# Optimization experiments

Hardware: AMD Instinct MI355X
Metric: run time of the kernel (lower is better)

Reference implementation:

```python
import jax, jax.numpy as jnp
import numpy as np

B, S, P = 2, 1024, 1024          # batch, new tokens, start_pos (cached prefix)
E, H, KV, HD = 2048, 32, 8, 64    # embed, heads, kv groups, head_dim
G = H // KV                       # group size = 4
THETA = 500000.0
CTX = P + S                       # cache/context length = 2048


def _rope_tables(start, seqlen):
    inv_freq = 1.0 / (THETA ** (jnp.arange(0, HD, 2, dtype=jnp.float32) / HD))
    pos = jnp.arange(start, start + seqlen, dtype=jnp.float32)
    freqs = jnp.outer(pos, inv_freq)              # [S, HD/2]
    emb = jnp.concatenate([freqs, freqs], axis=-1)  # [S, HD]
    return jnp.cos(emb), jnp.sin(emb)


def setup_inputs() -> dict:
    key = jax.random.key(0)
    ks = jax.random.split(key, 8)
    x = jax.random.normal(ks[0], (B, S, E), dtype=jnp.float32)
    cos1, sin1 = _rope_tables(P, S)
    cos = jnp.broadcast_to(cos1[None], (B, S, HD))
    sin = jnp.broadcast_to(sin1[None], (B, S, HD))
    # causal-with-offset additive mask: query i (global pos P+i) sees key j <= P+i
    qpos = P + jnp.arange(S)[:, None]
    kpos = jnp.arange(CTX)[None, :]
    mask = jnp.where(kpos <= qpos, 0.0, -1e9).astype(jnp.float32)[None, None]  # [1,1,S,CTX]
    cache_k = jax.random.normal(ks[1], (B, KV, CTX, HD), dtype=jnp.float32)
    cache_v = jax.random.normal(ks[2], (B, KV, CTX, HD), dtype=jnp.float32)
    sc = 0.02
    Wq = jax.random.normal(ks[3], (E, E), dtype=jnp.float32) * sc
    Wk = jax.random.normal(ks[4], (KV * HD, E), dtype=jnp.float32) * sc
    Wv = jax.random.normal(ks[5], (KV * HD, E), dtype=jnp.float32) * sc
    Wo = jax.random.normal(ks[6], (E, E), dtype=jnp.float32) * sc
    return {"x": x, "cos": cos, "sin": sin, "mask": mask,
            "cache_k": cache_k, "cache_v": cache_v,
            "Wq": Wq, "Wk": Wk, "Wv": Wv, "Wo": Wo, "start_pos": P}


def _rotate_half(t):
    t1, t2 = t[..., : HD // 2], t[..., HD // 2:]
    return jnp.concatenate([-t2, t1], axis=-1)


def _apply_rope(t, cos, sin):
    # t: [B, nh, S, HD]; cos/sin: [B, S, HD] -> unsqueeze head dim
    c = cos[:, None]
    s = sin[:, None]
    return t * c + _rotate_half(t) * s


def reference(x, cos, sin, mask, cache_k, cache_v, Wq, Wk, Wv, Wo, start_pos):
    b, s, e = x.shape
    q = (x @ Wq.T).reshape(b, s, H, HD).transpose(0, 2, 1, 3)    # [B,H,S,HD]
    k = (x @ Wk.T).reshape(b, s, KV, HD).transpose(0, 2, 1, 3)   # [B,KV,S,HD]
    v = (x @ Wv.T).reshape(b, s, KV, HD).transpose(0, 2, 1, 3)
    q = _apply_rope(q, cos, sin)
    k = _apply_rope(k, cos, sin)
    ck = cache_k.at[:, :, start_pos:start_pos + s].set(k)
    cv = cache_v.at[:, :, start_pos:start_pos + s].set(v)
    keys = ck[:, :, : start_pos + s]      # [B,KV,T,HD]
    vals = cv[:, :, : start_pos + s]
    # GQA without materializing repeated KV: view q as [B,KV,G,S,HD]
    qg = q.reshape(b, KV, G, s, HD)
    scores = jnp.einsum("bkgsh,bkth->bkgst", qg, keys) / jnp.sqrt(jnp.float32(HD))
    scores = scores + mask[:, :, None]    # broadcast mask over group dim
    probs = jax.nn.softmax(scores.astype(jnp.float32), axis=-1).astype(x.dtype)
    out = jnp.einsum("bkgst,bkth->bkgsh", probs, vals)            # [B,KV,G,S,HD]
    out = out.reshape(b, H, s, HD).transpose(0, 2, 1, 3).reshape(b, s, e)
    return out @ Wo.T
```

## Files before the change

### kernel.cpp

```cpp
#include <hip/hip_runtime.h>
#include <cstddef>

#define B   2
#define S   1024
#define PP  1024
#define CTX 2048
#define E   2048
#define H   32
#define KVH 8
#define HD  64
#define GQ  4
#define NQKV 3072

typedef short s4v  __attribute__((ext_vector_type(4)));
typedef short s8v  __attribute__((ext_vector_type(8)));
typedef float f4v  __attribute__((ext_vector_type(4)));

__device__ __forceinline__ short f2bf(float f) {
  union { float f; unsigned u; } v; v.f = f;
  unsigned r = v.u + 0x7fffu + ((v.u >> 16) & 1u);
  return (short)(r >> 16);
}
__device__ __forceinline__ float bf2f(short h) {
  union { unsigned u; float f; } v; v.u = ((unsigned)(unsigned short)h) << 16;
  return v.f;
}

__device__ __forceinline__ void gl_lds16(const void* g, void* l) {
  __builtin_amdgcn_global_load_lds((const __attribute__((address_space(1))) unsigned*)g,
                                   (__attribute__((address_space(3))) unsigned*)l, 16, 0, 0);
}

__global__ __launch_bounds__(256) void prep(const float* __restrict__ x,
                                            const float* __restrict__ Wq,
                                            const float* __restrict__ Wk,
                                            const float* __restrict__ Wv,
                                            const float* __restrict__ Wo,
                                            const float* __restrict__ ck,
                                            const float* __restrict__ cv,
                                            short* __restrict__ xb,
                                            short* __restrict__ wqkv,
                                            short* __restrict__ wob,
                                            short* __restrict__ keys,
                                            short* __restrict__ vt,
                                            float4* __restrict__ outz) {
  __shared__ short Ts[64][72];
  const int blk = blockIdx.x, tid = threadIdx.x;
  if (blk < 7168) {
    const float* s; short* d; int base;
    if (blk < 2048)      { s = x;  d = xb;             base = blk; }
    else if (blk < 4096) { s = Wq; d = wqkv;           base = blk - 2048; }
    else if (blk < 4608) { s = Wk; d = wqkv + 4194304; base = blk - 4096; }
    else if (blk < 5120) { s = Wv; d = wqkv + 5242880; base = blk - 4608; }
    else                 { s = Wo; d = wob;            base = blk - 5120; }
    int i = (base * 256 + tid) * 8;
    float4 a = *(const float4*)&s[i];
    float4 b = *(const float4*)&s[i + 4];
    s8v o;
    o[0]=f2bf(a.x); o[1]=f2bf(a.y); o[2]=f2bf(a.z); o[3]=f2bf(a.w);
    o[4]=f2bf(b.x); o[5]=f2bf(b.y); o[6]=f2bf(b.z); o[7]=f2bf(b.w);
    *(s8v*)&d[i] = o;
  } else if (blk < 7680) {
    int idx = (blk - 7168) * 256 + tid;
    int bkv = idx >> 13;
    int rem = idx & 8191;
    size_t off = (size_t)bkv * (CTX * HD) + (size_t)rem * 8;
    float4 a = *(const float4*)&ck[off];
    float4 b = *(const float4*)&ck[off + 4];
    s8v o;
    o[0]=f2bf(a.x); o[1]=f2bf(a.y); o[2]=f2bf(a.z); o[3]=f2bf(a.w);
    o[4]=f2bf(b.x); o[5]=f2bf(b.y); o[6]=f2bf(b.z); o[7]=f2bf(b.w);
    *(s8v*)&keys[off] = o;
  } else if (blk < 7936) {
    const int blk2 = blk - 7680;
    const int bkv = blk2 >> 4;
    const int p0  = (blk2 & 15) * 64;
    const float* src = cv + (size_t)bkv * CTX * HD + (size_t)p0 * HD;
    {
      int dq = tid & 15, kb = tid >> 4;
      float4 vv[4];
#pragma unroll
      for (int i = 0; i < 4; i++)
        vv[i] = *(const float4*)&src[(size_t)(kb * 4 + i) * HD + dq * 4];
#pragma unroll
      for (int j = 0; j < 4; j++) {
        s4v p;
        p[0]=f2bf(((const float*)&vv[0])[j]); p[1]=f2bf(((const float*)&vv[1])[j]);
        p[2]=f2bf(((const float*)&vv[2])[j]); p[3]=f2bf(((const float*)&vv[3])[j]);
        *(s4v*)&Ts[dq * 4 + j][kb * 4] = p;
      }
    }
    __syncthreads();
    {
      int d = tid >> 2, c = tid & 3;
      short* dst = vt + ((size_t)bkv * HD + d) * CTX + p0 + (c >> 1) * 32 + (c & 1) * 4;
#pragma unroll
      for (int j = 0; j < 4; j++) {
        s4v q4 = *(const s4v*)&Ts[d][c * 16 + j * 4];
        *(s4v*)&dst[j * 8] = q4;
      }
    }
  } else {
    int i0 = (blk - 7936) * 1024 + tid * 4;
#pragma unroll
    for (int j = 0; j < 4; j++) outz[i0 + j] = make_float4(0.f, 0.f, 0.f, 0.f);
  }
}

__global__ __launch_bounds__(256) void qkv_gemm(const short* __restrict__ A,
                                                const short* __restrict__ Bw,
                                                short* __restrict__ qb,
                                                short* __restrict__ ktmp,
                                                short* __restrict__ vt) {
  __shared__ short As[4096];
  __shared__ short Bs[4096];
  const int tid  = threadIdx.x;
  const int wv   = tid >> 6, lane = tid & 63;
  const int wm   = wv & 1, wn = wv >> 1;
  const int n16  = lane & 15, g = lane >> 4;
  const int m0   = blockIdx.y * 128, n0 = blockIdx.x * 128;
  const int K = 2048;

  const int s0 = tid, s1 = 256 + tid;
  const int r0 = s0 >> 2, c0 = ((s0 & 3) ^ ((r0 >> 1) & 3)) * 8;
  const int r1 = s1 >> 2, c1 = ((s1 & 3) ^ ((r1 >> 1) & 3)) * 8;
  const short* pA0 = A + (size_t)(m0 + r0) * K + c0;
  const short* pA1 = A + (size_t)(m0 + r1) * K + c1;
  const short* pB0 = Bw + (size_t)(n0 + r0) * K + c0;
  const short* pB1 = Bw + (size_t)(n0 + r1) * K + c1;
  short* lA0 = As + (wv * 64) * 8;
  short* lA1 = As + (256 + wv * 64) * 8;
  short* lB0 = Bs + (wv * 64) * 8;
  short* lB1 = Bs + (256 + wv * 64) * 8;

  const int xv = (g ^ ((n16 >> 1) & 3)) * 8;

  f4v acc[4][4] = {};
  for (int k0 = 0; k0 < K; k0 += 32) {
    __syncthreads();
    gl_lds16(pA0, lA0); gl_lds16(pA1, lA1);
    gl_lds16(pB0, lB0); gl_lds16(pB1, lB1);
    pA0 += 32; pA1 += 32; pB0 += 32; pB1 += 32;
    __syncthreads();

    s8v af[4], bf[4];
#pragma unroll
    for (int mt = 0; mt < 4; mt++)
      af[mt] = *(const s8v*)&As[(wm * 64 + mt * 16 + n16) * 32 + xv];
#pragma unroll
    for (int nt = 0; nt < 4; nt++)
      bf[nt] = *(const s8v*)&Bs[(wn * 64 + nt * 16 + n16) * 32 + xv];
#pragma unroll
    for (int mt = 0; mt < 4; mt++)
#pragma unroll
      for (int nt = 0; nt < 4; nt++)
        acc[mt][nt] = __builtin_amdgcn_mfma_f32_16x16x32_bf16(af[mt], bf[nt], acc[mt][nt], 0, 0, 0);
  }

  const int rowb = m0 + wm * 64 + g * 4;
  const int colb = n0 + wn * 64 + n16;
  if (n0 < 2048) {
#pragma unroll
    for (int mt = 0; mt < 4; mt++)
#pragma unroll
      for (int nt = 0; nt < 4; nt++) {
        size_t base = (size_t)(rowb + mt * 16) * E + colb + nt * 16;
#pragma unroll
        for (int r = 0; r < 4; r++)
          qb[base + (size_t)r * E] = f2bf(acc[mt][nt][r]);
      }
  } else if (n0 < 2560) {
#pragma unroll
    for (int mt = 0; mt < 4; mt++)
#pragma unroll
      for (int nt = 0; nt < 4; nt++) {
        size_t base = (size_t)(rowb + mt * 16) * 512 + colb - 2048 + nt * 16;
#pragma unroll
        for (int r = 0; r < 4; r++)
          ktmp[base + (size_t)r * 512] = f2bf(acc[mt][nt][r]);
      }
  } else {
    const int b    = m0 >> 10;
    const int head = ((n0 - 2560) >> 6) + wn;
    const int sbase = (m0 - (b << 10)) + wm * 64;
    const size_t vrowb = (size_t)(b * KVH + head) * HD;
#pragma unroll
    for (int mt = 0; mt < 4; mt++) {
      const int pos = PP + sbase + ((mt >> 1) << 5) + ((mt & 1) << 2) + (g << 3);
#pragma unroll
      for (int nt = 0; nt < 4; nt++) {
        const int d = nt * 16 + n16;
        s4v o;
        o[0] = f2bf(acc[mt][nt][0]); o[1] = f2bf(acc[mt][nt][1]);
        o[2] = f2bf(acc[mt][nt][2]); o[3] = f2bf(acc[mt][nt][3]);
        *(s4v*)&vt[(vrowb + d) * CTX + pos] = o;
      }
    }
  }
}

__global__ __launch_bounds__(256) void gemm_bf16_sk(const short* __restrict__ A,
                                                    const short* __restrict__ Bw,
                                                    float* __restrict__ C,
                                                    int M, int N, int K) {
  __shared__ short As[4096];
  __shared__ short Bs[4096];
  const int tid  = threadIdx.x;
  const int wv   = tid >> 6, lane = tid & 63;
  const int wm   = wv & 1, wn = wv >> 1;
  const int n16  = lane & 15, g = lane >> 4;
  const int m0   = blockIdx.y * 128, n0 = blockIdx.x * 128;
  const int kh   = K >> 1;
  const int kbeg = blockIdx.z * kh;

  const int s0 = tid, s1 = 256 + tid;
  const int r0 = s0 >> 2, c0 = ((s0 & 3) ^ ((r0 >> 1) & 3)) * 8;
  const int r1 = s1 >> 2, c1 = ((s1 & 3) ^ ((r1 >> 1) & 3)) * 8;
  const short* pA0 = A + (size_t)(m0 + r0) * K + kbeg + c0;
  const short* pA1 = A + (size_t)(m0 + r1) * K + kbeg + c1;
  const short* pB0 = Bw + (size_t)(n0 + r0) * K + kbeg + c0;
  const short* pB1 = Bw + (size_t)(n0 + r1) * K + kbeg + c1;
  short* lA0 = As + (wv * 64) * 8;
  short* lA1 = As + (256 + wv * 64) * 8;
  short* lB0 = Bs + (wv * 64) * 8;
  short* lB1 = Bs + (256 + wv * 64) * 8;

  const int xv = (g ^ ((n16 >> 1) & 3)) * 8;

  f4v acc[4][4] = {};
  for (int k0 = 0; k0 < kh; k0 += 32) {
    __syncthreads();
    gl_lds16(pA0, lA0); gl_lds16(pA1, lA1);
    gl_lds16(pB0, lB0); gl_lds16(pB1, lB1);
    pA0 += 32; pA1 += 32; pB0 += 32; pB1 += 32;
    __syncthreads();

    s8v af[4], bf[4];
#pragma unroll
    for (int mt = 0; mt < 4; mt++)
      af[mt] = *(const s8v*)&As[(wm * 64 + mt * 16 + n16) * 32 + xv];
#pragma unroll
    for (int nt = 0; nt < 4; nt++)
      bf[nt] = *(const s8v*)&Bs[(wn * 64 + nt * 16 + n16) * 32 + xv];
#pragma unroll
    for (int mt = 0; mt < 4; mt++)
#pragma unroll
      for (int nt = 0; nt < 4; nt++)
        acc[mt][nt] = __builtin_amdgcn_mfma_f32_16x16x32_bf16(af[mt], bf[nt], acc[mt][nt], 0, 0, 0);
  }

#pragma unroll
  for (int mt = 0; mt < 4; mt++)
#pragma unroll
    for (int nt = 0; nt < 4; nt++) {
      size_t base = (size_t)(m0 + wm * 64 + mt * 16 + g * 4) * N + n0 + wn * 64 + nt * 16 + n16;
#pragma unroll
      for (int r = 0; r < 4; r++)
        unsafeAtomicAdd(&C[base + (size_t)r * N], acc[mt][nt][r]);
    }
}

__global__ __launch_bounds__(256) void rope_kb(const short* __restrict__ ktmp,
                                               const float* __restrict__ cosb,
                                               const float* __restrict__ sinb,
                                               short* __restrict__ keys) {
  int idx = blockIdx.x * 256 + threadIdx.x;
  int d = idx & 31;
  int kv = (idx >> 5) & (KVH - 1);
  int s = (idx >> 8) & (S - 1);
  int b = idx >> 18;
  size_t row = (size_t)b * S + s;
  float c = cosb[row * HD + d];
  float sn = sinb[row * HD + d];
  float k1 = bf2f(ktmp[row * 512 + kv * 64 + d]);
  float k2 = bf2f(ktmp[row * 512 + kv * 64 + d + 32]);
  size_t drow = (((size_t)b * KVH + kv) * CTX + PP + s) * HD;
  keys[drow + d]      = f2bf(k1 * c - k2 * sn);
  keys[drow + d + 32] = f2bf(k2 * c + k1 * sn);
}

__global__ __launch_bounds__(256) void attn_mfma(const short* __restrict__ qb,
                                                 const float* __restrict__ cosb,
                                                 const float* __restrict__ sinb,
                                                 const short* __restrict__ keys,
                                                 const short* __restrict__ valsT,
                                                 short* __restrict__ attn) {
  __shared__ short Ks[4096];
  __shared__ short VTs[4096];

  const int sblk = 15 - (blockIdx.x & 15);
  const int h    = (blockIdx.x >> 4) & (H - 1);
  const int b    = blockIdx.x >> 9;
  const int kv   = h >> 2;
  const int sq0  = sblk * 64;
  const int kend = PP + sq0 + 64;

  const int tid  = threadIdx.x;
  const int w    = tid >> 6;
  const int lane = tid & 63;
  const int n    = lane & 15;
  const int g    = lane >> 4;

  const short* kbase = keys  + ((size_t)b * KVH + kv) * CTX * HD;
  const short* vtb   = valsT + ((size_t)b * KVH + kv) * (size_t)HD * CTX;

  union { s4v h4[2]; s8v v; } qlo, qhi;
  {
    const size_t row = (size_t)b * S + sq0 + w * 16 + n;
    const short* qrow = qb + row * E + h * 64;
    const float* crow = cosb + row * HD;
    const float* srow = sinb + row * HD;
    const float SC = 0.18033688011112042f;
    s8v q0 = *(const s8v*)&qrow[g * 8];
    s8v q1 = *(const s8v*)&qrow[32 + g * 8];
    float cc[8], ss[8];
    *(float4*)&cc[0] = *(const float4*)&crow[g * 8];
    *(float4*)&cc[4] = *(const float4*)&crow[g * 8 + 4];
    *(float4*)&ss[0] = *(const float4*)&srow[g * 8];
    *(float4*)&ss[4] = *(const float4*)&srow[g * 8 + 4];
#pragma unroll
    for (int j = 0; j < 8; j++) {
      float fl = bf2f(q0[j]), fh = bf2f(q1[j]);
      qlo.v[j] = f2bf((fl * cc[j] - fh * ss[j]) * SC);
      qhi.v[j] = f2bf((fh * cc[j] + fl * ss[j]) * SC);
    }
  }

  f4v O[4] = {{0,0,0,0},{0,0,0,0},{0,0,0,0},{0,0,0,0}};
  float la[4] = {0.f, 0.f, 0.f, 0.f};
  const int qp     = PP + sq0 + w * 16 + n;
  const int qmin_w = PP + sq0 + w * 16;

  const int lrow = lane >> 3;
  const int sw   = (lane & 7) ^ lrow;
  const short* kg0 = kbase + (size_t)(w * 8 + lrow) * HD + sw * 8;
  const short* kg1 = kg0 + 32 * HD;
  const short* vg0 = vtb + (size_t)(w * 8 + lrow) * CTX + sw * 8;
  const short* vg1 = vg0 + (size_t)32 * CTX;
  short* kl0 = Ks + w * 512;
  short* kl1 = Ks + 2048 + w * 512;
  short* vl0 = VTs + w * 512;
  short* vl1 = VTs + 2048 + w * 512;

  const int xsl = (g ^ (n & 7)) * 8;

  for (int k0 = 0; k0 < kend; k0 += 64) {
    __syncthreads();
    gl_lds16(kg0 + (size_t)k0 * HD, kl0);
    gl_lds16(kg1 + (size_t)k0 * HD, kl1);
    gl_lds16(vg0 + k0, vl0);
    gl_lds16(vg1 + k0, vl1);
    __syncthreads();

    if (k0 >= qmin_w + 16) continue;

    f4v sc[4];
#pragma unroll
    for (int st = 0; st < 4; st++) {
      const short* krow = &Ks[(st * 16 + n) * 64];
      s8v alo = *(const s8v*)(krow + xsl);
      s8v ahi = *(const s8v*)(krow + (xsl ^ 32));
      f4v z = {0.f, 0.f, 0.f, 0.f};
      z = __builtin_amdgcn_mfma_f32_16x16x32_bf16(alo, qlo.v, z, 0, 0, 0);
      sc[st] = __builtin_amdgcn_mfma_f32_16x16x32_bf16(ahi, qhi.v, z, 0, 0, 0);
    }

    if (k0 + 63 > qmin_w) {
#pragma unroll
      for (int st = 0; st < 4; st++)
#pragma unroll
        for (int r = 0; r < 4; r++) {
          int kpos = k0 + st * 16 + g * 4 + r;
          if (kpos > qp) sc[st][r] = -3e38f;
        }
    }

    union { unsigned u[4]; s8v v; } pb0, pb1;
#pragma unroll
    for (int st = 0; st < 4; st++) {
      float e0 = __builtin_amdgcn_exp2f(sc[st][0]);
      float e1 = __builtin_amdgcn_exp2f(sc[st][1]);
      float e2 = __builtin_amdgcn_exp2f(sc[st][2]);
      float e3 = __builtin_amdgcn_exp2f(sc[st][3]);
      la[0] += e0; la[1] += e1; la[2] += e2; la[3] += e3;
      unsigned w0, w1;
      asm("v_cvt_pk_bf16_f32 %0, %1, %2" : "=v"(w0) : "v"(e0), "v"(e1));
      asm("v_cvt_pk_bf16_f32 %0, %1, %2" : "=v"(w1) : "v"(e2), "v"(e3));
      if (st < 2) { pb0.u[st * 2] = w0; pb0.u[st * 2 + 1] = w1; }
      else        { pb1.u[(st - 2) * 2] = w0; pb1.u[(st - 2) * 2 + 1] = w1; }
    }

#pragma unroll
    for (int dg = 0; dg < 4; dg++) {
      const short* vr = &VTs[(dg * 16 + n) * 64];
      s8v va = *(const s8v*)(vr + xsl);
      s8v vb = *(const s8v*)(vr + (xsl ^ 32));
      O[dg] = __builtin_amdgcn_mfma_f32_16x16x32_bf16(va, pb0.v, O[dg], 0, 0, 0);
      O[dg] = __builtin_amdgcn_mfma_f32_16x16x32_bf16(vb, pb1.v, O[dg], 0, 0, 0);
    }
  }

  float l = (la[0] + la[1]) + (la[2] + la[3]);
  l += __shfl_xor(l, 16);
  l += __shfl_xor(l, 32);
  const float rl = 1.f / l;
  short* orow = attn + ((size_t)b * S + sq0 + w * 16 + n) * E + h * 64;
#pragma unroll
  for (int dg = 0; dg < 4; dg++) {
    s4v o;
    o[0] = f2bf(O[dg][0] * rl); o[1] = f2bf(O[dg][1] * rl);
    o[2] = f2bf(O[dg][2] * rl); o[3] = f2bf(O[dg][3] * rl);
    *(s4v*)&orow[dg * 16 + g * 4] = o;
  }
}

extern "C" void kernel_launch(void* const* d_in, const int* in_sizes, int n_in,
                              void* d_out, int out_size, void* d_ws, size_t ws_size,
                              hipStream_t stream) {
  const float* x       = (const float*)d_in[0];
  const float* cosb    = (const float*)d_in[1];
  const float* sinb    = (const float*)d_in[2];
  const float* cache_k = (const float*)d_in[4];
  const float* cache_v = (const float*)d_in[5];
  const float* Wq      = (const float*)d_in[6];
  const float* Wk      = (const float*)d_in[7];
  const float* Wv      = (const float*)d_in[8];
  const float* Wo      = (const float*)d_in[9];
  float* out = (float*)d_out;

  short* xb    = (short*)d_ws;
  short* wqkv  = xb + 4194304;
  short* wob   = wqkv + 6291456;
  short* keysb = wob + 4194304;
  short* valsT = keysb + 2097152;
  short* aout  = valsT + 2097152;
  short* qb    = aout + 4194304;
  short* ktmp  = qb + 4194304;

  dim3 blk(256);

  prep<<<8960, blk, 0, stream>>>(x, Wq, Wk, Wv, Wo, cache_k, cache_v,
                                 xb, wqkv, wob, keysb, valsT, (float4*)out);

  qkv_gemm<<<dim3(NQKV / 128, (B * S) / 128), blk, 0, stream>>>(xb, wqkv, qb, ktmp, valsT);

  rope_kb<<<(B * S * KVH * 32) / 256, blk, 0, stream>>>(ktmp, cosb, sinb, keysb);

  attn_mfma<<<B * H * (S / 64), blk, 0, stream>>>(qb, cosb, sinb, keysb, valsT, aout);

  gemm_bf16_sk<<<dim3(E / 128, (B * S) / 128, 2), blk, 0, stream>>>(aout, wob, out, B * S, E, E);
}
```

Measured before the change: 276.5 us.

## Pair complementary query blocks per attention block and double-buffer K/V staging

Each attention workgroup now handles two query tiles, a late one and an early one (15-pr and pr), so causal work per block is balanced and each staged K/V tile in LDS serves both tiles. K/V loads move to a double-buffered LDS scheme that prefetches the next tile while the current one is computed, leaving one barrier per iteration. The grid halves to 512 blocks, and register and LDS use roughly double, which may cut occupancy.

```diff
diff --git a/kernel.cpp b/kernel.cpp
--- a/kernel.cpp
+++ b/kernel.cpp
@@ -285,15 +285,16 @@
                                                  const short* __restrict__ keys,
                                                  const short* __restrict__ valsT,
                                                  short* __restrict__ attn) {
-  __shared__ short Ks[4096];
-  __shared__ short VTs[4096];
-
-  const int sblk = 15 - (blockIdx.x & 15);
-  const int h    = (blockIdx.x >> 4) & (H - 1);
-  const int b    = blockIdx.x >> 9;
-  const int kv   = h >> 2;
-  const int sq0  = sblk * 64;
-  const int kend = PP + sq0 + 64;
+  __shared__ short Ks[8192];
+  __shared__ short VTs[8192];
+
+  const int pr = blockIdx.x & 7;
+  const int h  = (blockIdx.x >> 3) & (H - 1);
+  const int b  = blockIdx.x >> 8;
+  const int kv = h >> 2;
+  const int sqA = (15 - pr) * 64;
+  const int sqB = pr * 64;
+  const int kendA = PP + sqA + 64;
 
   const int tid  = threadIdx.x;
   const int w    = tid >> 6;
@@ -304,8 +305,11 @@
   const short* kbase = keys  + ((size_t)b * KVH + kv) * CTX * HD;
   const short* vtb   = valsT + ((size_t)b * KVH + kv) * (size_t)HD * CTX;
 
-  union { s4v h4[2]; s8v v; } qlo, qhi;
-  {
+  union qfrag { s4v h4[2]; s8v v; };
+  union pu    { unsigned u[4]; s8v v; };
+
+  qfrag qloA, qhiA, qloB, qhiB;
+  auto load_q = [&](int sq0, qfrag& qlo, qfrag& qhi) {
     const size_t row = (size_t)b * S + sq0 + w * 16 + n;
     const short* qrow = qb + row * E + h * 64;
     const float* crow = cosb + row * HD;
@@ -324,12 +328,16 @@
       qlo.v[j] = f2bf((fl * cc[j] - fh * ss[j]) * SC);
       qhi.v[j] = f2bf((fh * cc[j] + fl * ss[j]) * SC);
     }
-  }
-
-  f4v O[4] = {{0,0,0,0},{0,0,0,0},{0,0,0,0},{0,0,0,0}};
-  float la[4] = {0.f, 0.f, 0.f, 0.f};
-  const int qp     = PP + sq0 + w * 16 + n;
-  const int qmin_w = PP + sq0 + w * 16;
+  };
+  load_q(sqA, qloA, qhiA);
+  load_q(sqB, qloB, qhiB);
+
+  f4v OA[4] = {{0,0,0,0},{0,0,0,0},{0,0,0,0},{0,0,0,0}};
+  f4v OB[4] = {{0,0,0,0},{0,0,0,0},{0,0,0,0},{0,0,0,0}};
+  float laA[4] = {0.f,0.f,0.f,0.f};
+  float laB[4] = {0.f,0.f,0.f,0.f};
+  const int qpA = PP + sqA + w * 16 + n, qminA = PP + sqA + w * 16;
+  const int qpB = PP + sqB + w * 16 + n, qminB = PP + sqB + w * 16;
 
   const int lrow = lane >> 3;
   const int sw   = (lane & 7) ^ lrow;
@@ -337,45 +345,27 @@
   const short* kg1 = kg0 + 32 * HD;
   const short* vg0 = vtb + (size_t)(w * 8 + lrow) * CTX + sw * 8;
   const short* vg1 = vg0 + (size_t)32 * CTX;
-  short* kl0 = Ks + w * 512;
-  short* kl1 = Ks + 2048 + w * 512;
-  short* vl0 = VTs + w * 512;
-  short* vl1 = VTs + 2048 + w * 512;
-
-  const int xsl = (g ^ (n & 7)) * 8;
-
-  for (int k0 = 0; k0 < kend; k0 += 64) {
-    __syncthreads();
-    gl_lds16(kg0 + (size_t)k0 * HD, kl0);
-    gl_lds16(kg1 + (size_t)k0 * HD, kl1);
-    gl_lds16(vg0 + k0, vl0);
-    gl_lds16(vg1 + k0, vl1);
-    __syncthreads();
-
-    if (k0 >= qmin_w + 16) continue;
-
-    f4v sc[4];
-#pragma unroll
-    for (int st = 0; st < 4; st++) {
-      const short* krow = &Ks[(st * 16 + n) * 64];
-      s8v alo = *(const s8v*)(krow + xsl);
-      s8v ahi = *(const s8v*)(krow + (xsl ^ 32));
-      f4v z = {0.f, 0.f, 0.f, 0.f};
-      z = __builtin_amdgcn_mfma_f32_16x16x32_bf16(alo, qlo.v, z, 0, 0, 0);
-      sc[st] = __builtin_amdgcn_mfma_f32_16x16x32_bf16(ahi, qhi.v, z, 0, 0, 0);
-    }
-
-    if (k0 + 63 > qmin_w) {
-#pragma unroll
-      for (int st = 0; st < 4; st++)
-#pragma unroll
-        for (int r = 0; r < 4; r++) {
-          int kpos = k0 + st * 16 + g * 4 + r;
-          if (kpos > qp) sc[st][r] = -3e38f;
-        }
-    }
-
-    union { unsigned u[4]; s8v v; } pb0, pb1;
+
+  auto stage = [&](int buf, int k0) {
+    short* kl = Ks  + buf * 4096 + w * 512;
+    short* vl = VTs + buf * 4096 + w * 512;
+    gl_lds16(kg0 + (size_t)k0 * HD, kl);
+    gl_lds16(kg1 + (size_t)k0 * HD, kl + 2048);
+    gl_lds16(vg0 + k0, vl);
+    gl_lds16(vg1 + k0, vl + 2048);
+  };
+
+  auto mask_diag = [&](f4v (&sc)[4], int k0, int qp) {
+#pragma unroll
+    for (int st = 0; st < 4; st++)
+#pragma unroll
+      for (int r = 0; r < 4; r++) {
+        int kpos = k0 + st * 16 + g * 4 + r;
+        if (kpos > qp) sc[st][r] = -3e38f;
+      }
+  };
+
+  auto softmax_pack = [&](f4v (&sc)[4], float (&la)[4], pu& p0, pu& p1) {
 #pragma unroll
     for (int st = 0; st < 4; st++) {
       float e0 = __builtin_amdgcn_exp2f(sc[st][0]);
@@ -386,32 +376,79 @@
       unsigned w0, w1;
       asm("v_cvt_pk_bf16_f32 %0, %1, %2" : "=v"(w0) : "v"(e0), "v"(e1));
       asm("v_cvt_pk_bf16_f32 %0, %1, %2" : "=v"(w1) : "v"(e2), "v"(e3));
-      if (st < 2) { pb0.u[st * 2] = w0; pb0.u[st * 2 + 1] = w1; }
-      else        { pb1.u[(st - 2) * 2] = w0; pb1.u[(st - 2) * 2 + 1] = w1; }
-    }
-
+      if (st < 2) { p0.u[st * 2] = w0; p0.u[st * 2 + 1] = w1; }
+      else        { p1.u[(st - 2) * 2] = w0; p1.u[(st - 2) * 2 + 1] = w1; }
+    }
+  };
+
+  const int xsl = (g ^ (n & 7)) * 8;
+
+  stage(0, 0);
+  int cur = 0;
+  for (int k0 = 0; k0 < kendA; k0 += 64) {
+    __syncthreads();
+    if (k0 + 64 < kendA) stage(cur ^ 1, k0 + 64);
+
+    if (k0 < qminA + 16) {
+      const bool doB = (k0 < qminB + 16);
+      const short* kb = &Ks[cur * 4096];
+      const short* vb = &VTs[cur * 4096];
+
+      f4v scA[4], scB[4];
+#pragma unroll
+      for (int st = 0; st < 4; st++) {
+        const short* krow = kb + (st * 16 + n) * 64;
+        s8v alo = *(const s8v*)(krow + xsl);
+        s8v ahi = *(const s8v*)(krow + (xsl ^ 32));
+        f4v z = {0.f, 0.f, 0.f, 0.f};
+        z = __builtin_amdgcn_mfma_f32_16x16x32_bf16(alo, qloA.v, z, 0, 0, 0);
+        scA[st] = __builtin_amdgcn_mfma_f32_16x16x32_bf16(ahi, qhiA.v, z, 0, 0, 0);
+        if (doB) {
+          f4v zb = {0.f, 0.f, 0.f, 0.f};
+          zb = __builtin_amdgcn_mfma_f32_16x16x32_bf16(alo, qloB.v, zb, 0, 0, 0);
+          scB[st] = __builtin_amdgcn_mfma_f32_16x16x32_bf16(ahi, qhiB.v, zb, 0, 0, 0);
+        }
+      }
+
+      if (k0 + 63 > qminA) mask_diag(scA, k0, qpA);
+      if (doB && k0 + 63 > qminB) mask_diag(scB, k0, qpB);
+
+      pu pb0A, pb1A, pb0B, pb1B;
+      softmax_pack(scA, laA, pb0A, pb1A);
+      if (doB) softmax_pack(scB, laB, pb0B, pb1B);
+
+#pragma unroll
+      for (int dg = 0; dg < 4; dg++) {
+        const short* vr = vb + (dg * 16 + n) * 64;
+        s8v va = *(const s8v*)(vr + xsl);
+        s8v vx = *(const s8v*)(vr + (xsl ^ 32));
+        OA[dg] = __builtin_amdgcn_mfma_f32_16x16x32_bf16(va, pb0A.v, OA[dg], 0, 0, 0);
+        OA[dg] = __builtin_amdgcn_mfma_f32_16x16x32_bf16(vx, pb1A.v, OA[dg], 0, 0, 0);
+        if (doB) {
+          OB[dg] = __builtin_amdgcn_mfma_f32_16x16x32_bf16(va, pb0B.v, OB[dg], 0, 0, 0);
+          OB[dg] = __builtin_amdgcn_mfma_f32_16x16x32_bf16(vx, pb1B.v, OB[dg], 0, 0, 0);
+        }
+      }
+    }
+    cur ^= 1;
+  }
+
+  auto finish = [&](f4v (&O)[4], float (&la)[4], int sq0) {
+    float l = (la[0] + la[1]) + (la[2] + la[3]);
+    l += __shfl_xor(l, 16);
+    l += __shfl_xor(l, 32);
+    const float rl = 1.f / l;
+    short* orow = attn + ((size_t)b * S + sq0 + w * 16 + n) * E + h * 64;
 #pragma unroll
     for (int dg = 0; dg < 4; dg++) {
-      const short* vr = &VTs[(dg * 16 + n) * 64];
-      s8v va = *(const s8v*)(vr + xsl);
-      s8v vb = *(const s8v*)(vr + (xsl ^ 32));
-      O[dg] = __builtin_amdgcn_mfma_f32_16x16x32_bf16(va, pb0.v, O[dg], 0, 0, 0);
-      O[dg] = __builtin_amdgcn_mfma_f32_16x16x32_bf16(vb, pb1.v, O[dg], 0, 0, 0);
-    }
-  }
-
-  float l = (la[0] + la[1]) + (la[2] + la[3]);
-  l += __shfl_xor(l, 16);
-  l += __shfl_xor(l, 32);
-  const float rl = 1.f / l;
-  short* orow = attn + ((size_t)b * S + sq0 + w * 16 + n) * E + h * 64;
-#pragma unroll
-  for (int dg = 0; dg < 4; dg++) {
-    s4v o;
-    o[0] = f2bf(O[dg][0] * rl); o[1] = f2bf(O[dg][1] * rl);
-    o[2] = f2bf(O[dg][2] * rl); o[3] = f2bf(O[dg][3] * rl);
-    *(s4v*)&orow[dg * 16 + g * 4] = o;
-  }
+      s4v o;
+      o[0] = f2bf(O[dg][0] * rl); o[1] = f2bf(O[dg][1] * rl);
+      o[2] = f2bf(O[dg][2] * rl); o[3] = f2bf(O[dg][3] * rl);
+      *(s4v*)&orow[dg * 16 + g * 4] = o;
+    }
+  };
+  finish(OA, laA, sqA);
+  finish(OB, laB, sqB);
 }
 
 extern "C" void kernel_launch(void* const* d_in, const int* in_sizes, int n_in,
@@ -446,7 +483,7 @@
 
   rope_kb<<<(B * S * KVH * 32) / 256, blk, 0, stream>>>(ktmp, cosb, sinb, keysb);
 
-  attn_mfma<<<B * H * (S / 64), blk, 0, stream>>>(qb, cosb, sinb, keysb, valsT, aout);
+  attn_mfma<<<B * H * 8, blk, 0, stream>>>(qb, cosb, sinb, keysb, valsT, aout);
 
   gemm_bf16_sk<<<dim3(E / 128, (B * S) / 128, 2), blk, 0, stream>>>(aout, wob, out, B * S, E, E);
 }
```

Result: slower. 284.5 us (+2.9%).

## Double-buffer K/V tiles in attention and widen GEMM K-tile to 64

Applied to the files above, without the earlier changes.

The attention kernel now keeps two LDS buffers for the K and V^T tiles. It prefetches the next 64-key tile while computing on the current one, which removes one barrier per iteration and lets the global-to-LDS copy overlap with the MFMA and softmax work. Both bf16 GEMMs (QKV projection and split-K output projection) now step 64 along K instead of 32. The LDS tiles and the XOR swizzle are reorganised to match, which halves the number of barriers per unit of work. The cost is double the LDS use in all three kernels, which may lower occupancy.

```diff
diff --git a/kernel.cpp b/kernel.cpp
--- a/kernel.cpp
+++ b/kernel.cpp
@@ -112,8 +112,8 @@
                                                 short* __restrict__ qb,
                                                 short* __restrict__ ktmp,
                                                 short* __restrict__ vt) {
-  __shared__ short As[4096];
-  __shared__ short Bs[4096];
+  __shared__ short As[8192];
+  __shared__ short Bs[8192];
   const int tid  = threadIdx.x;
   const int wv   = tid >> 6, lane = tid & 63;
   const int wm   = wv & 1, wn = wv >> 1;
@@ -121,40 +121,37 @@
   const int m0   = blockIdx.y * 128, n0 = blockIdx.x * 128;
   const int K = 2048;
 
-  const int s0 = tid, s1 = 256 + tid;
-  const int r0 = s0 >> 2, c0 = ((s0 & 3) ^ ((r0 >> 1) & 3)) * 8;
-  const int r1 = s1 >> 2, c1 = ((s1 & 3) ^ ((r1 >> 1) & 3)) * 8;
-  const short* pA0 = A + (size_t)(m0 + r0) * K + c0;
-  const short* pA1 = A + (size_t)(m0 + r1) * K + c1;
-  const short* pB0 = Bw + (size_t)(n0 + r0) * K + c0;
-  const short* pB1 = Bw + (size_t)(n0 + r1) * K + c1;
-  short* lA0 = As + (wv * 64) * 8;
-  short* lA1 = As + (256 + wv * 64) * 8;
-  short* lB0 = Bs + (wv * 64) * 8;
-  short* lB1 = Bs + (256 + wv * 64) * 8;
-
-  const int xv = (g ^ ((n16 >> 1) & 3)) * 8;
+  const int rr = tid >> 3;
+  const int cc = ((tid & 7) ^ (rr & 7)) * 8;
+  const short* pA = A  + (size_t)(m0 + rr) * K + cc;
+  const short* pB = Bw + (size_t)(n0 + rr) * K + cc;
 
   f4v acc[4][4] = {};
-  for (int k0 = 0; k0 < K; k0 += 32) {
-    __syncthreads();
-    gl_lds16(pA0, lA0); gl_lds16(pA1, lA1);
-    gl_lds16(pB0, lB0); gl_lds16(pB1, lB1);
-    pA0 += 32; pA1 += 32; pB0 += 32; pB1 += 32;
-    __syncthreads();
-
-    s8v af[4], bf[4];
-#pragma unroll
-    for (int mt = 0; mt < 4; mt++)
-      af[mt] = *(const s8v*)&As[(wm * 64 + mt * 16 + n16) * 32 + xv];
-#pragma unroll
-    for (int nt = 0; nt < 4; nt++)
-      bf[nt] = *(const s8v*)&Bs[(wn * 64 + nt * 16 + n16) * 32 + xv];
-#pragma unroll
-    for (int mt = 0; mt < 4; mt++)
+  for (int k0 = 0; k0 < K; k0 += 64) {
+    __syncthreads();
+#pragma unroll
+    for (int st = 0; st < 4; st++) {
+      gl_lds16(pA + (size_t)st * 32 * K, As + (st * 256 + wv * 64) * 8);
+      gl_lds16(pB + (size_t)st * 32 * K, Bs + (st * 256 + wv * 64) * 8);
+    }
+    pA += 64; pB += 64;
+    __syncthreads();
+
+#pragma unroll
+    for (int kk = 0; kk < 2; kk++) {
+      s8v af[4], bf[4];
+#pragma unroll
+      for (int mt = 0; mt < 4; mt++)
+        af[mt] = *(const s8v*)&As[(wm * 64 + mt * 16 + n16) * 64 + (((kk << 2) | g) ^ (n16 & 7)) * 8];
 #pragma unroll
       for (int nt = 0; nt < 4; nt++)
-        acc[mt][nt] = __builtin_amdgcn_mfma_f32_16x16x32_bf16(af[mt], bf[nt], acc[mt][nt], 0, 0, 0);
+        bf[nt] = *(const s8v*)&Bs[(wn * 64 + nt * 16 + n16) * 64 + (((kk << 2) | g) ^ (n16 & 7)) * 8];
+#pragma unroll
+      for (int mt = 0; mt < 4; mt++)
+#pragma unroll
+        for (int nt = 0; nt < 4; nt++)
+          acc[mt][nt] = __builtin_amdgcn_mfma_f32_16x16x32_bf16(af[mt], bf[nt], acc[mt][nt], 0, 0, 0);
+    }
   }
 
   const int rowb = m0 + wm * 64 + g * 4;
@@ -203,8 +200,8 @@
                                                     const short* __restrict__ Bw,
                                                     float* __restrict__ C,
                                                     int M, int N, int K) {
-  __shared__ short As[4096];
-  __shared__ short Bs[4096];
+  __shared__ short As[8192];
+  __shared__ short Bs[8192];
   const int tid  = threadIdx.x;
   const int wv   = tid >> 6, lane = tid & 63;
   const int wm   = wv & 1, wn = wv >> 1;
@@ -213,40 +210,37 @@
   const int kh   = K >> 1;
   const int kbeg = blockIdx.z * kh;
 
-  const int s0 = tid, s1 = 256 + tid;
-  const int r0 = s0 >> 2, c0 = ((s0 & 3) ^ ((r0 >> 1) & 3)) * 8;
-  const int r1 = s1 >> 2, c1 = ((s1 & 3) ^ ((r1 >> 1) & 3)) * 8;
-  const short* pA0 = A + (size_t)(m0 + r0) * K + kbeg + c0;
-  const short* pA1 = A + (size_t)(m0 + r1) * K + kbeg + c1;
-  const short* pB0 = Bw + (size_t)(n0 + r0) * K + kbeg + c0;
-  const short* pB1 = Bw + (size_t)(n0 + r1) * K + kbeg + c1;
-  short* lA0 = As + (wv * 64) * 8;
-  short* lA1 = As + (256 + wv * 64) * 8;
-  short* lB0 = Bs + (wv * 64) * 8;
-  short* lB1 = Bs + (256 + wv * 64) * 8;
-
-  const int xv = (g ^ ((n16 >> 1) & 3)) * 8;
+  const int rr = tid >> 3;
+  const int cc = ((tid & 7) ^ (rr & 7)) * 8;
+  const short* pA = A  + (size_t)(m0 + rr) * K + kbeg + cc;
+  const short* pB = Bw + (size_t)(n0 + rr) * K + kbeg + cc;
 
   f4v acc[4][4] = {};
-  for (int k0 = 0; k0 < kh; k0 += 32) {
-    __syncthreads();
-    gl_lds16(pA0, lA0); gl_lds16(pA1, lA1);
-    gl_lds16(pB0, lB0); gl_lds16(pB1, lB1);
-    pA0 += 32; pA1 += 32; pB0 += 32; pB1 += 32;
-    __syncthreads();
-
-    s8v af[4], bf[4];
-#pragma unroll
-    for (int mt = 0; mt < 4; mt++)
-      af[mt] = *(const s8v*)&As[(wm * 64 + mt * 16 + n16) * 32 + xv];
-#pragma unroll
-    for (int nt = 0; nt < 4; nt++)
-      bf[nt] = *(const s8v*)&Bs[(wn * 64 + nt * 16 + n16) * 32 + xv];
-#pragma unroll
-    for (int mt = 0; mt < 4; mt++)
+  for (int k0 = 0; k0 < kh; k0 += 64) {
+    __syncthreads();
+#pragma unroll
+    for (int st = 0; st < 4; st++) {
+      gl_lds16(pA + (size_t)st * 32 * K, As + (st * 256 + wv * 64) * 8);
+      gl_lds16(pB + (size_t)st * 32 * K, Bs + (st * 256 + wv * 64) * 8);
+    }
+    pA += 64; pB += 64;
+    __syncthreads();
+
+#pragma unroll
+    for (int kk = 0; kk < 2; kk++) {
+      s8v af[4], bf[4];
+#pragma unroll
+      for (int mt = 0; mt < 4; mt++)
+        af[mt] = *(const s8v*)&As[(wm * 64 + mt * 16 + n16) * 64 + (((kk << 2) | g) ^ (n16 & 7)) * 8];
 #pragma unroll
       for (int nt = 0; nt < 4; nt++)
-        acc[mt][nt] = __builtin_amdgcn_mfma_f32_16x16x32_bf16(af[mt], bf[nt], acc[mt][nt], 0, 0, 0);
+        bf[nt] = *(const s8v*)&Bs[(wn * 64 + nt * 16 + n16) * 64 + (((kk << 2) | g) ^ (n16 & 7)) * 8];
+#pragma unroll
+      for (int mt = 0; mt < 4; mt++)
+#pragma unroll
+        for (int nt = 0; nt < 4; nt++)
+          acc[mt][nt] = __builtin_amdgcn_mfma_f32_16x16x32_bf16(af[mt], bf[nt], acc[mt][nt], 0, 0, 0);
+    }
   }
 
 #pragma unroll
@@ -285,8 +279,8 @@
                                                  const short* __restrict__ keys,
                                                  const short* __restrict__ valsT,
                                                  short* __restrict__ attn) {
-  __shared__ short Ks[4096];
-  __shared__ short VTs[4096];
+  __shared__ short Ks[8192];
+  __shared__ short VTs[8192];
 
   const int sblk = 15 - (blockIdx.x & 15);
   const int h    = (blockIdx.x >> 4) & (H - 1);
@@ -337,67 +331,81 @@
   const short* kg1 = kg0 + 32 * HD;
   const short* vg0 = vtb + (size_t)(w * 8 + lrow) * CTX + sw * 8;
   const short* vg1 = vg0 + (size_t)32 * CTX;
-  short* kl0 = Ks + w * 512;
-  short* kl1 = Ks + 2048 + w * 512;
-  short* vl0 = VTs + w * 512;
-  short* vl1 = VTs + 2048 + w * 512;
 
   const int xsl = (g ^ (n & 7)) * 8;
 
+  {
+    short* kl = Ks  + w * 512;
+    short* vl = VTs + w * 512;
+    gl_lds16(kg0, kl);
+    gl_lds16(kg1, kl + 2048);
+    gl_lds16(vg0, vl);
+    gl_lds16(vg1, vl + 2048);
+  }
+
+  int cur = 0;
   for (int k0 = 0; k0 < kend; k0 += 64) {
     __syncthreads();
-    gl_lds16(kg0 + (size_t)k0 * HD, kl0);
-    gl_lds16(kg1 + (size_t)k0 * HD, kl1);
-    gl_lds16(vg0 + k0, vl0);
-    gl_lds16(vg1 + k0, vl1);
-    __syncthreads();
-
-    if (k0 >= qmin_w + 16) continue;
-
-    f4v sc[4];
-#pragma unroll
-    for (int st = 0; st < 4; st++) {
-      const short* krow = &Ks[(st * 16 + n) * 64];
-      s8v alo = *(const s8v*)(krow + xsl);
-      s8v ahi = *(const s8v*)(krow + (xsl ^ 32));
-      f4v z = {0.f, 0.f, 0.f, 0.f};
-      z = __builtin_amdgcn_mfma_f32_16x16x32_bf16(alo, qlo.v, z, 0, 0, 0);
-      sc[st] = __builtin_amdgcn_mfma_f32_16x16x32_bf16(ahi, qhi.v, z, 0, 0, 0);
-    }
-
-    if (k0 + 63 > qmin_w) {
-#pragma unroll
-      for (int st = 0; st < 4; st++)
-#pragma unroll
-        for (int r = 0; r < 4; r++) {
-          int kpos = k0 + st * 16 + g * 4 + r;
-          if (kpos > qp) sc[st][r] = -3e38f;
-        }
-    }
-
-    union { unsigned u[4]; s8v v; } pb0, pb1;
-#pragma unroll
-    for (int st = 0; st < 4; st++) {
-      float e0 = __builtin_amdgcn_exp2f(sc[st][0]);
-      float e1 = __builtin_amdgcn_exp2f(sc[st][1]);
-      float e2 = __builtin_amdgcn_exp2f(sc[st][2]);
-      float e3 = __builtin_amdgcn_exp2f(sc[st][3]);
-      la[0] += e0; la[1] += e1; la[2] += e2; la[3] += e3;
-      unsigned w0, w1;
-      asm("v_cvt_pk_bf16_f32 %0, %1, %2" : "=v"(w0) : "v"(e0), "v"(e1));
-      asm("v_cvt_pk_bf16_f32 %0, %1, %2" : "=v"(w1) : "v"(e2), "v"(e3));
-      if (st < 2) { pb0.u[st * 2] = w0; pb0.u[st * 2 + 1] = w1; }
-      else        { pb1.u[(st - 2) * 2] = w0; pb1.u[(st - 2) * 2 + 1] = w1; }
-    }
-
-#pragma unroll
-    for (int dg = 0; dg < 4; dg++) {
-      const short* vr = &VTs[(dg * 16 + n) * 64];
-      s8v va = *(const s8v*)(vr + xsl);
-      s8v vb = *(const s8v*)(vr + (xsl ^ 32));
-      O[dg] = __builtin_amdgcn_mfma_f32_16x16x32_bf16(va, pb0.v, O[dg], 0, 0, 0);
-      O[dg] = __builtin_amdgcn_mfma_f32_16x16x32_bf16(vb, pb1.v, O[dg], 0, 0, 0);
-    }
+    if (k0 + 64 < kend) {
+      const int kn = k0 + 64;
+      short* kl = Ks  + (cur ^ 1) * 4096 + w * 512;
+      short* vl = VTs + (cur ^ 1) * 4096 + w * 512;
+      gl_lds16(kg0 + (size_t)kn * HD, kl);
+      gl_lds16(kg1 + (size_t)kn * HD, kl + 2048);
+      gl_lds16(vg0 + kn, vl);
+      gl_lds16(vg1 + kn, vl + 2048);
+    }
+
+    if (k0 < qmin_w + 16) {
+      const short* kb = &Ks[cur * 4096];
+      const short* vb = &VTs[cur * 4096];
+
+      f4v sc[4];
+#pragma unroll
+      for (int st = 0; st < 4; st++) {
+        const short* krow = kb + (st * 16 + n) * 64;
+        s8v alo = *(const s8v*)(krow + xsl);
+        s8v ahi = *(const s8v*)(krow + (xsl ^ 32));
+        f4v z = {0.f, 0.f, 0.f, 0.f};
+        z = __builtin_amdgcn_mfma_f32_16x16x32_bf16(alo, qlo.v, z, 0, 0, 0);
+        sc[st] = __builtin_amdgcn_mfma_f32_16x16x32_bf16(ahi, qhi.v, z, 0, 0, 0);
+      }
+
+      if (k0 + 63 > qmin_w) {
+#pragma unroll
+        for (int st = 0; st < 4; st++)
+#pragma unroll
+          for (int r = 0; r < 4; r++) {
+            int kpos = k0 + st * 16 + g * 4 + r;
+            if (kpos > qp) sc[st][r] = -3e38f;
+          }
+      }
+
+      union { unsigned u[4]; s8v v; } pb0, pb1;
+#pragma unroll
+      for (int st = 0; st < 4; st++) {
+        float e0 = __builtin_amdgcn_exp2f(sc[st][0]);
+        float e1 = __builtin_amdgcn_exp2f(sc[st][1]);
+        float e2 = __builtin_amdgcn_exp2f(sc[st][2]);
+        float e3 = __builtin_amdgcn_exp2f(sc[st][3]);
+        la[0] += e0; la[1] += e1; la[2] += e2; la[3] += e3;
+        unsigned w0, w1;
+        asm("v_cvt_pk_bf16_f32 %0, %1, %2" : "=v"(w0) : "v"(e0), "v"(e1));
+        asm("v_cvt_pk_bf16_f32 %0, %1, %2" : "=v"(w1) : "v"(e2), "v"(e3));
+        if (st < 2) { pb0.u[st * 2] = w0; pb0.u[st * 2 + 1] = w1; }
+        else        { pb1.u[(st - 2) * 2] = w0; pb1.u[(st - 2) * 2 + 1] = w1; }
+      }
+
+#pragma unroll
+      for (int dg = 0; dg < 4; dg++) {
+        const short* vr = vb + (dg * 16 + n) * 64;
+        s8v va = *(const s8v*)(vr + xsl);
+        s8v vx = *(const s8v*)(vr + (xsl ^ 32));
+        O[dg] = __builtin_amdgcn_mfma_f32_16x16x32_bf16(va, pb0.v, O[dg], 0, 0, 0);
+        O[dg] = __builtin_amdgcn_mfma_f32_16x16x32_bf16(vx, pb1.v, O[dg], 0, 0, 0);
+      }
+    }
+    cur ^= 1;
   }
 
   float l = (la[0] + la[1]) + (la[2] + la[3]);
```

New measurement: 270.8 us. -2.1%, faster.
